# Kernel tuning notes

Hardware: AMD Instinct MI355X
Metric: run time of the kernel (lower is better)

## Reference

```python
import jax, jax.numpy as jnp
import numpy as np

E, H, FFN, NQ, NL = 1024, 16, 4096, 8, 4
LN_EPS = 1e-5


def _rx(t):
    c = jnp.cos(t / 2).astype(jnp.complex64)
    s = (-1j * jnp.sin(t / 2)).astype(jnp.complex64)
    return jnp.stack([jnp.stack([c, s]), jnp.stack([s, c])])


def _ry(t):
    c = jnp.cos(t / 2).astype(jnp.complex64)
    s = jnp.sin(t / 2).astype(jnp.complex64)
    return jnp.stack([jnp.stack([c, -s]), jnp.stack([s, c])])


def _rz(t):
    tc = t.astype(jnp.complex64)
    e0 = jnp.exp(-1j * tc / 2)
    e1 = jnp.exp(1j * tc / 2)
    z = jnp.zeros((), jnp.complex64)
    return jnp.stack([jnp.stack([e0, z]), jnp.stack([z, e1])])


def _apply_1q(state, gate, q):
    state = jnp.tensordot(gate, state, axes=([1], [q]))
    return jnp.moveaxis(state, 0, q)


def _cnot(state, c, t):
    s0, s1 = jnp.split(state, 2, axis=c)  # each keeps size-1 axis c
    s1 = jnp.flip(s1, axis=t)            # X on target when control=1
    return jnp.concatenate([s0, s1], axis=c)


def quantum_expvals(qparams):
    # statevector sim of the fixed (input-independent) variational circuit
    state = jnp.zeros((2,) * NQ, jnp.complex64).at[(0,) * NQ].set(1.0)
    for l in range(NL):
        for q in range(NQ):
            state = _apply_1q(state, _rx(qparams[l, q, 0]), q)
            state = _apply_1q(state, _ry(qparams[l, q, 1]), q)
            state = _apply_1q(state, _rz(qparams[l, q, 2]), q)
        for i in range(NQ - 1):
            state = _cnot(state, i, i + 1)
        state = _cnot(state, NQ - 1, 0)
    probs = jnp.abs(state) ** 2
    evs = [1.0 - 2.0 * jnp.sum(jnp.take(probs, 1, axis=q)) for q in range(NQ)]
    return jnp.stack(evs).astype(jnp.float32)  # [NQ]


def _layernorm(x, g, b):
    m = jnp.mean(x, axis=-1, keepdims=True)
    v = jnp.mean((x - m) ** 2, axis=-1, keepdims=True)
    return (x - m) / jnp.sqrt(v + LN_EPS) * g + b


def setup_inputs() -> dict:
    key = jax.random.key(0)
    ks = jax.random.split(key, 16)
    s = 1.0 / np.sqrt(E)
    inp = {
        "x": jax.random.normal(ks[0], (4, 1024, E), jnp.float32),
        "Wq": jax.random.normal(ks[1], (E, E), jnp.float32) * s,
        "Wk": jax.random.normal(ks[2], (E, E), jnp.float32) * s,
        "Wv": jax.random.normal(ks[3], (E, E), jnp.float32) * s,
        "Wo": jax.random.normal(ks[4], (E, E), jnp.float32) * s,
        "bo": jnp.zeros((E,), jnp.float32),
        "gate": jnp.ones((H,), jnp.float32),
        "g1": jnp.ones((E,), jnp.float32),
        "b1": jnp.zeros((E,), jnp.float32),
        "g2": jnp.ones((E,), jnp.float32),
        "b2": jnp.zeros((E,), jnp.float32),
        "Wi": jax.random.normal(ks[5], (NQ, E), jnp.float32) * s,
        "bi": jnp.zeros((NQ,), jnp.float32),
        "qparams": jax.random.normal(ks[6], (NL, NQ, 3), jnp.float32),
        "W1": jax.random.normal(ks[7], (FFN, NQ), jnp.float32) / np.sqrt(NQ),
        "bf1": jnp.zeros((FFN,), jnp.float32),
        "W2": jax.random.normal(ks[8], (E, FFN), jnp.float32) / np.sqrt(FFN),
        "bf2": jnp.zeros((E,), jnp.float32),
    }
    return inp


def reference(x, Wq, Wk, Wv, Wo, bo, gate, g1, b1, g2, b2, Wi, bi, qparams, W1, bf1, W2, bf2):
    B, T, _ = x.shape
    d_k = E // H
    # gated multi-head attention (dropout = identity / eval mode)
    q = (x @ Wq.T).reshape(B, T, H, d_k)
    k = (x @ Wk.T).reshape(B, T, H, d_k)
    v = (x @ Wv.T).reshape(B, T, H, d_k)
    scores = jnp.einsum("bqhd,bkhd->bhqk", q, k) / np.sqrt(d_k)
    attn = jax.nn.softmax(scores, axis=-1)
    out = jnp.einsum("bhqk,bkhd->bqhd", attn, v)
    out = out * jax.nn.sigmoid(gate)[None, None, :, None]
    attn_out = out.reshape(B, T, E) @ Wo.T + bo
    h = _layernorm(x + attn_out, g1, b1)
    # quantum FFN: input_linear output is computed but unused by the circuit
    h2d = h.reshape(B * T, E)
    _x_qubits = h2d @ Wi.T + bi  # faithfully computed, unused (as in original)
    evs = quantum_expvals(qparams)                      # [NQ], token-independent
    qout = jnp.broadcast_to(evs, (B * T, NQ))
    f = jax.nn.relu(qout @ W1.T + bf1) @ W2.T + bf2     # [B*T, E]
    ffn_out = f.reshape(B, T, E)
    return _layernorm(h + ffn_out, g2, b2)
```

## Files before the change

kernel.cpp:

```cpp
#include <hip/hip_runtime.h>

#define E_DIM 1024
#define SEQ 1024
#define BATCH 4
#define NHEAD 16
#define DK 64
#define TOK 4096
#define FFN_DIM 4096
#define NQB 8
#define NLAY 4

typedef __attribute__((ext_vector_type(8))) short short8;
typedef __attribute__((ext_vector_type(4))) float f32x4;
typedef unsigned short u16;
typedef unsigned int u32;

__device__ __forceinline__ u16 f2bf(float f) {
  union { float f; unsigned u; } v; v.f = f;
  unsigned r = v.u + 0x7fffu + ((v.u >> 16) & 1u);
  return (u16)(r >> 16);
}

__device__ __forceinline__ u32 cvtpk_bf16(float lo, float hi) {
  u32 r;
  asm("v_cvt_pk_bf16_f32 %0, %1, %2" : "=v"(r) : "v"(lo), "v"(hi));
  return r;
}

__device__ __forceinline__ void gload_lds16(const u16* g, u16* l) {
  __builtin_amdgcn_global_load_lds((const __attribute__((address_space(1))) unsigned int*)g,
                                   (__attribute__((address_space(3))) unsigned int*)l, 16, 0, 0);
}

__global__ void cast_kernel(const float* __restrict__ in, u16* __restrict__ out, int n4) {
  int i = blockIdx.x * blockDim.x + threadIdx.x;
  int stride = gridDim.x * blockDim.x;
  for (; i < n4; i += stride) {
    float4 v = ((const float4*)in)[i];
    ushort4 o;
    o.x = f2bf(v.x); o.y = f2bf(v.y); o.z = f2bf(v.z); o.w = f2bf(v.w);
    ((ushort4*)out)[i] = o;
  }
}

__global__ void cast4_kernel(const float* __restrict__ a0, const float* __restrict__ a1,
                             const float* __restrict__ a2, const float* __restrict__ a3,
                             u16* __restrict__ out, int n4per) {
  const float* src = blockIdx.z == 0 ? a0 : blockIdx.z == 1 ? a1 : blockIdx.z == 2 ? a2 : a3;
  u16* dst = out + (size_t)blockIdx.z * n4per * 4;
  int i = blockIdx.x * blockDim.x + threadIdx.x;
  int stride = gridDim.x * blockDim.x;
  for (; i < n4per; i += stride) {
    float4 v = ((const float4*)src)[i];
    ushort4 o;
    o.x = f2bf(v.x); o.y = f2bf(v.y); o.z = f2bf(v.z); o.w = f2bf(v.w);
    ((ushort4*)dst)[i] = o;
  }
}

template<int F32OUT, int ZTRANS>
__global__ __launch_bounds__(256) void gemm_bt(
    const u16* __restrict__ A,
    const u16* __restrict__ B0, const u16* __restrict__ B1, const u16* __restrict__ B2,
    void* __restrict__ C0, void* __restrict__ C1, void* __restrict__ C2,
    const float* __restrict__ bias, int K, int N) {
  const u16* B = blockIdx.z == 0 ? B0 : blockIdx.z == 1 ? B1 : B2;
  void* C = blockIdx.z == 0 ? C0 : blockIdx.z == 1 ? C1 : C2;
  __shared__ u16 As[128 * 32];
  __shared__ u16 Bs[128 * 32];
  const int tid = threadIdx.x;
  const int lane = tid & 63;
  const int wid = tid >> 6;
  const int wr = wid >> 1, wc = wid & 1;
  const int lr = lane & 15, lg = lane >> 4;
  const int row0 = blockIdx.y * 128;
  const int col0 = blockIdx.x * 128;
  const int ar = tid >> 2;
  const int ak = (tid & 3) * 8;
  const u16* Ag = A + (size_t)(row0 + ar) * K + ak;
  const u16* Bg = B + (size_t)(col0 + ar) * K + ak;
  u16* AsW = &As[wid * 512];
  u16* BsW = &Bs[wid * 512];
  f32x4 acc[4][4];
  const f32x4 fzero = {0.f, 0.f, 0.f, 0.f};
#pragma unroll
  for (int m = 0; m < 4; ++m)
#pragma unroll
    for (int n = 0; n < 4; ++n) acc[m][n] = fzero;
  for (int k0 = 0; k0 < K; k0 += 32) {
    __syncthreads();
    gload_lds16(Ag + k0, AsW);
    gload_lds16(Ag + (size_t)64 * K + k0, AsW + 2048);
    gload_lds16(Bg + k0, BsW);
    gload_lds16(Bg + (size_t)64 * K + k0, BsW + 2048);
    __syncthreads();
    short8 af[4], bfr[4];
#pragma unroll
    for (int m = 0; m < 4; ++m) af[m] = *(const short8*)&As[(wr * 64 + m * 16 + lr) * 32 + lg * 8];
#pragma unroll
    for (int n = 0; n < 4; ++n) bfr[n] = *(const short8*)&Bs[(wc * 64 + n * 16 + lr) * 32 + lg * 8];
#pragma unroll
    for (int m = 0; m < 4; ++m)
#pragma unroll
      for (int n = 0; n < 4; ++n)
        acc[m][n] = __builtin_amdgcn_mfma_f32_16x16x32_bf16(af[m], bfr[n], acc[m][n], 0, 0, 0);
  }
#pragma unroll
  for (int m = 0; m < 4; ++m) {
    const int growb = row0 + wr * 64 + m * 16 + lg * 4;
#pragma unroll
    for (int n = 0; n < 4; ++n) {
      const int gcol = col0 + wc * 64 + n * 16 + lr;
      if (ZTRANS >= 0 && blockIdx.z == ZTRANS) {
        ushort4 t4;
        t4.x = f2bf(acc[m][n][0]); t4.y = f2bf(acc[m][n][1]);
        t4.z = f2bf(acc[m][n][2]); t4.w = f2bf(acc[m][n][3]);
        *(ushort4*)&((u16*)C)[(size_t)gcol * TOK + growb] = t4;
      } else {
#pragma unroll
        for (int r = 0; r < 4; ++r) {
          size_t idx = (size_t)(growb + r) * N + gcol;
          if (F32OUT) ((float*)C)[idx] = acc[m][n][r] + bias[gcol];
          else ((u16*)C)[idx] = f2bf(acc[m][n][r]);
        }
      }
    }
  }
}

__global__ __launch_bounds__(256) void attn_kernel(
    const u16* __restrict__ qb, const u16* __restrict__ kb, const u16* __restrict__ vtb,
    const float* __restrict__ gate, u16* __restrict__ ob) {
  const int bid = blockIdx.x + (blockIdx.y << 4) + (blockIdx.z << 8);
  const int swz = (bid & 7) * 128 + (bid >> 3);
  const int qblk = swz & 15, h = (swz >> 4) & 15, b = swz >> 8;
  const int tid = threadIdx.x, lane = tid & 63, w = tid >> 6;
  const int lr = lane & 15, lg = lane >> 4;
  __shared__ u16 Kl[2][64 * 64];
  __shared__ u16 Vl[2][64 * 64];
  const u16* Qp = qb + (size_t)(b * SEQ + qblk * 64 + w * 16 + lr) * E_DIM + h * DK;
  const short8 bq0 = *(const short8*)&Qp[lg * 8];
  const short8 bq1 = *(const short8*)&Qp[32 + lg * 8];
  const int r0 = tid >> 3;
  const int cs = (tid & 7) ^ (r0 & 7);
  const u16* Kg0 = kb + (size_t)(b * SEQ + r0) * E_DIM + h * DK + cs * 8;
  const u16* Kg1 = Kg0 + (size_t)32 * E_DIM;
  const u16* Vg0 = vtb + (size_t)(h * DK + r0) * TOK + b * SEQ + cs * 8;
  const u16* Vg1 = Vg0 + (size_t)32 * TOK;
  const int ldsb = w * 512;
#define STAGE(bufi, kt) do { \
    const size_t ko = (size_t)(kt) * 64 * E_DIM; const int vo = (kt) * 64; \
    gload_lds16(Kg0 + ko, &Kl[bufi][ldsb]); \
    gload_lds16(Kg1 + ko, &Kl[bufi][2048 + ldsb]); \
    gload_lds16(Vg0 + vo, &Vl[bufi][ldsb]); \
    gload_lds16(Vg1 + vo, &Vl[bufi][2048 + ldsb]); \
  } while (0)
  f32x4 o[4];
  const f32x4 fzero = {0.f, 0.f, 0.f, 0.f};
#pragma unroll
  for (int dn = 0; dn < 4; ++dn) o[dn] = fzero;
  float mrun = -1e30f, lrun = 0.f;
  const int sw = (lr & 7) << 3;
  const int srcA = ((lg & 1) << 5) + lr;
  const bool hi = (lg & 2) != 0;
  STAGE(0, 0);
  __syncthreads();
  int cur = 0;
  for (int kt = 0; kt < 16; ++kt) {
    if (kt < 15) STAGE(cur ^ 1, kt + 1);
    const u16* Kc = Kl[cur];
    const u16* Vc = Vl[cur];
    f32x4 sT[4];
#pragma unroll
    for (int n = 0; n < 4; ++n) {
      const int base = (n * 16 + lr) * 64;
      const short8 ka0 = *(const short8*)&Kc[base + ((lg << 3) ^ sw)];
      const short8 ka1 = *(const short8*)&Kc[base + ((32 + (lg << 3)) ^ sw)];
      sT[n] = __builtin_amdgcn_mfma_f32_16x16x32_bf16(ka0, bq0, fzero, 0, 0, 0);
      sT[n] = __builtin_amdgcn_mfma_f32_16x16x32_bf16(ka1, bq1, sT[n], 0, 0, 0);
    }
    float mt = sT[0][0];
#pragma unroll
    for (int n = 0; n < 4; ++n)
#pragma unroll
      for (int r = 0; r < 4; ++r) mt = fmaxf(mt, sT[n][r]);
    mt = fmaxf(mt, __shfl_xor(mt, 16));
    mt = fmaxf(mt, __shfl_xor(mt, 32));
    const float mn = fmaxf(mrun, mt * 0.125f);
    const float alpha = __expf(mrun - mn);
    mrun = mn;
    float tsum = 0.f;
    u32 pk[4][2];
#pragma unroll
    for (int n = 0; n < 4; ++n) {
      const float p0 = __expf(sT[n][0] * 0.125f - mn);
      const float p1 = __expf(sT[n][1] * 0.125f - mn);
      const float p2 = __expf(sT[n][2] * 0.125f - mn);
      const float p3 = __expf(sT[n][3] * 0.125f - mn);
      tsum += (p0 + p1) + (p2 + p3);
      pk[n][0] = cvtpk_bf16(p0, p1);
      pk[n][1] = cvtpk_bf16(p2, p3);
    }
    tsum += __shfl_xor(tsum, 16);
    tsum += __shfl_xor(tsum, 32);
    lrun = lrun * alpha + tsum;
#pragma unroll
    for (int dn = 0; dn < 4; ++dn)
#pragma unroll
      for (int r = 0; r < 4; ++r) o[dn][r] *= alpha;
#pragma unroll
    for (int kh = 0; kh < 2; ++kh) {
      const int nb = kh * 2;
      union { short8 s8; u32 d[4]; } pf;
      const u32 a0 = (u32)__shfl((int)pk[nb][0], srcA);
      const u32 c0 = (u32)__shfl((int)pk[nb + 1][0], srcA);
      const u32 a1 = (u32)__shfl((int)pk[nb][1], srcA);
      const u32 c1 = (u32)__shfl((int)pk[nb + 1][1], srcA);
      const u32 a2 = (u32)__shfl((int)pk[nb][0], srcA + 16);
      const u32 c2 = (u32)__shfl((int)pk[nb + 1][0], srcA + 16);
      const u32 a3 = (u32)__shfl((int)pk[nb][1], srcA + 16);
      const u32 c3 = (u32)__shfl((int)pk[nb + 1][1], srcA + 16);
      pf.d[0] = hi ? c0 : a0;
      pf.d[1] = hi ? c1 : a1;
      pf.d[2] = hi ? c2 : a2;
      pf.d[3] = hi ? c3 : a3;
#pragma unroll
      for (int dn = 0; dn < 4; ++dn) {
        const int base = (dn * 16 + lr) * 64;
        const short8 va = *(const short8*)&Vc[base + ((((kh * 4 + lg) << 3)) ^ sw)];
        o[dn] = __builtin_amdgcn_mfma_f32_16x16x32_bf16(va, pf.s8, o[dn], 0, 0, 0);
      }
    }
    __syncthreads();
    cur ^= 1;
  }
  const float sg = 1.f / (1.f + __expf(-gate[h]));
  const float inv = sg / lrun;
  const size_t orow = (size_t)(b * SEQ + qblk * 64 + w * 16 + lr) * E_DIM + h * DK;
#pragma unroll
  for (int dn = 0; dn < 4; ++dn) {
    ushort4 o4;
    o4.x = f2bf(o[dn][0] * inv);
    o4.y = f2bf(o[dn][1] * inv);
    o4.z = f2bf(o[dn][2] * inv);
    o4.w = f2bf(o[dn][3] * inv);
    *(ushort4*)&ob[orow + dn * 16 + lg * 4] = o4;
  }
#undef STAGE
}

__global__ __launch_bounds__(256) void quantum_kernel(
    const float* __restrict__ qparams, const float* __restrict__ W1,
    const float* __restrict__ bf1, float* __restrict__ relu_out) {
  __shared__ float csl[96], snl[96];
  __shared__ float evs_s[NQB];
  const int t = threadIdx.x;
  if (t < NLAY * NQB * 3) {
    const float th = qparams[t] * 0.5f;
    csl[t] = cosf(th);
    snl[t] = sinf(th);
  }
  __syncthreads();
  if (t < 64) {
    const int lane = t;
    float2 a[4];
    a[0] = make_float2(lane == 0 ? 1.f : 0.f, 0.f);
    a[1] = make_float2(0.f, 0.f);
    a[2] = make_float2(0.f, 0.f);
    a[3] = make_float2(0.f, 0.f);
#pragma unroll
    for (int l = 0; l < NLAY; ++l) {
#pragma unroll
      for (int q = 0; q < NQB; ++q) {
        const int pi = (l * NQB + q) * 3;
        const float cx = csl[pi],     sx = snl[pi];
        const float cy = csl[pi + 1], sy = snl[pi + 1];
        const float cz = csl[pi + 2], sz = snl[pi + 2];
        if (q < 6) {
          const int m = 1 << (5 - q);
          const int b = (lane >> (5 - q)) & 1;
#pragma unroll
          for (int r = 0; r < 4; ++r) {
            const float px = __shfl_xor(a[r].x, m);
            const float py = __shfl_xor(a[r].y, m);
            a[r] = make_float2(cx * a[r].x + sx * py, cx * a[r].y - sx * px);
          }
          const float sgy = b ? sy : -sy;
#pragma unroll
          for (int r = 0; r < 4; ++r) {
            const float px = __shfl_xor(a[r].x, m);
            const float py = __shfl_xor(a[r].y, m);
            a[r] = make_float2(cy * a[r].x + sgy * px, cy * a[r].y + sgy * py);
          }
          const float sgz = b ? -sz : sz;
#pragma unroll
          for (int r = 0; r < 4; ++r)
            a[r] = make_float2(cz * a[r].x + sgz * a[r].y, cz * a[r].y - sgz * a[r].x);
        } else if (q == 6) {
#pragma unroll
          for (int r = 0; r < 2; ++r) {
            float2 lo = a[r], hiv = a[r + 2];
            a[r]     = make_float2(cx * lo.x + sx * hiv.y, cx * lo.y - sx * hiv.x);
            a[r + 2] = make_float2(cx * hiv.x + sx * lo.y, cx * hiv.y - sx * lo.x);
          }
#pragma unroll
          for (int r = 0; r < 2; ++r) {
            float2 lo = a[r], hiv = a[r + 2];
            a[r]     = make_float2(cy * lo.x - sy * hiv.x, cy * lo.y - sy * hiv.y);
            a[r + 2] = make_float2(sy * lo.x + cy * hiv.x, sy * lo.y + cy * hiv.y);
          }
#pragma unroll
          for (int r = 0; r < 2; ++r) {
            float2 lo = a[r], hiv = a[r + 2];
            a[r]     = make_float2(cz * lo.x + sz * lo.y, cz * lo.y - sz * lo.x);
            a[r + 2] = make_float2(cz * hiv.x - sz * hiv.y, cz * hiv.y + sz * hiv.x);
          }
        } else {
#pragma unroll
          for (int r = 0; r < 4; r += 2) {
            float2 lo = a[r], hiv = a[r + 1];
            a[r]     = make_float2(cx * lo.x + sx * hiv.y, cx * lo.y - sx * hiv.x);
            a[r + 1] = make_float2(cx * hiv.x + sx * lo.y, cx * hiv.y - sx * lo.x);
          }
#pragma unroll
          for (int r = 0; r < 4; r += 2) {
            float2 lo = a[r], hiv = a[r + 1];
            a[r]     = make_float2(cy * lo.x - sy * hiv.x, cy * lo.y - sy * hiv.y);
            a[r + 1] = make_float2(sy * lo.x + cy * hiv.x, sy * lo.y + cy * hiv.y);
          }
#pragma unroll
          for (int r = 0; r < 4; r += 2) {
            float2 lo = a[r], hiv = a[r + 1];
            a[r]     = make_float2(cz * lo.x + sz * lo.y, cz * lo.y - sz * lo.x);
            a[r + 1] = make_float2(cz * hiv.x - sz * hiv.y, cz * hiv.y + sz * hiv.x);
          }
        }
      }
#pragma unroll
      for (int i = 0; i < 5; ++i) {
        const int cbit = 5 - i;
        const int tmask = 1 << (4 - i);
        const int ctrl = (lane >> cbit) & 1;
#pragma unroll
        for (int r = 0; r < 4; ++r) {
          const float px = __shfl_xor(a[r].x, tmask);
          const float py = __shfl_xor(a[r].y, tmask);
          if (ctrl) a[r] = make_float2(px, py);
        }
      }
      if (lane & 1) {
        float2 t0 = a[0]; a[0] = a[2]; a[2] = t0;
        float2 t1 = a[1]; a[1] = a[3]; a[3] = t1;
      }
      { float2 tt = a[2]; a[2] = a[3]; a[3] = tt; }
      a[1].x = __shfl_xor(a[1].x, 32); a[1].y = __shfl_xor(a[1].y, 32);
      a[3].x = __shfl_xor(a[3].x, 32); a[3].y = __shfl_xor(a[3].y, 32);
    }
    const float p0 = a[0].x * a[0].x + a[0].y * a[0].y;
    const float p1 = a[1].x * a[1].x + a[1].y * a[1].y;
    const float p2 = a[2].x * a[2].x + a[2].y * a[2].y;
    const float p3 = a[3].x * a[3].x + a[3].y * a[3].y;
    const float ptot = (p0 + p1) + (p2 + p3);
    float ev[8];
#pragma unroll
    for (int q = 0; q < 6; ++q) ev[q] = ((lane >> (5 - q)) & 1) ? ptot : 0.f;
    ev[6] = p2 + p3;
    ev[7] = p1 + p3;
#pragma unroll
    for (int d = 1; d < 64; d <<= 1)
#pragma unroll
      for (int q = 0; q < 8; ++q) ev[q] += __shfl_xor(ev[q], d);
    if (lane == 0) {
#pragma unroll
      for (int q = 0; q < 8; ++q) evs_s[q] = 1.f - 2.f * ev[q];
    }
  }
  __syncthreads();
  float e0 = evs_s[0], e1 = evs_s[1], e2 = evs_s[2], e3 = evs_s[3];
  float e4 = evs_s[4], e5 = evs_s[5], e6 = evs_s[6], e7 = evs_s[7];
  for (int j = t; j < FFN_DIM; j += 256) {
    const float4 w0 = *(const float4*)&W1[j * NQB];
    const float4 w1 = *(const float4*)&W1[j * NQB + 4];
    float acc = bf1[j];
    acc += e0 * w0.x + e1 * w0.y + e2 * w0.z + e3 * w0.w;
    acc += e4 * w1.x + e5 * w1.y + e6 * w1.z + e7 * w1.w;
    relu_out[j] = fmaxf(acc, 0.f);
  }
}

__global__ __launch_bounds__(256) void fvec_kernel(
    const float* __restrict__ W2, const float* __restrict__ bf2,
    const float* __restrict__ relu_vec, float* __restrict__ fvec) {
  const int w = threadIdx.x >> 6, lane = threadIdx.x & 63;
  const int e = blockIdx.x * 4 + w;
  const float* row = W2 + (size_t)e * FFN_DIM;
  float s = 0.f;
  for (int i = lane * 4; i < FFN_DIM; i += 256) {
    const float4 wv = *(const float4*)&row[i];
    const float4 rv = *(const float4*)&relu_vec[i];
    s += wv.x * rv.x + wv.y * rv.y + wv.z * rv.z + wv.w * rv.w;
  }
#pragma unroll
  for (int d = 32; d >= 1; d >>= 1) s += __shfl_down(s, d);
  if (lane == 0) fvec[e] = s + bf2[e];
}

__global__ __launch_bounds__(256) void final_ln_kernel(
    const float* __restrict__ x, const float* __restrict__ ao, const float* __restrict__ fvec,
    const float* __restrict__ g1, const float* __restrict__ b1,
    const float* __restrict__ g2, const float* __restrict__ b2, float* __restrict__ out) {
  __shared__ float sm1[8];
  __shared__ float sm2[8];
  const size_t row = blockIdx.x;
  const int tid = threadIdx.x;
  const int w = tid >> 6, lane = tid & 63;
  const float4 xv = *(const float4*)&x[row * E_DIM + tid * 4];
  const float4 av = *(const float4*)&ao[row * E_DIM + tid * 4];
  float v0 = xv.x + av.x, v1 = xv.y + av.y, v2 = xv.z + av.z, v3 = xv.w + av.w;
  float s = v0 + v1 + v2 + v3;
  float ss = v0 * v0 + v1 * v1 + v2 * v2 + v3 * v3;
#pragma unroll
  for (int d = 32; d >= 1; d >>= 1) { s += __shfl_down(s, d); ss += __shfl_down(ss, d); }
  if (lane == 0) { sm1[w * 2] = s; sm1[w * 2 + 1] = ss; }
  __syncthreads();
  s = sm1[0] + sm1[2] + sm1[4] + sm1[6];
  ss = sm1[1] + sm1[3] + sm1[5] + sm1[7];
  const float mean = s * (1.f / 1024.f);
  const float var = ss * (1.f / 1024.f) - mean * mean;
  const float rstd = rsqrtf(var + 1e-5f);
  const float4 g1v = *(const float4*)&g1[tid * 4];
  const float4 b1v = *(const float4*)&b1[tid * 4];
  const float4 fv = *(const float4*)&fvec[tid * 4];
  float z0 = (v0 - mean) * rstd * g1v.x + b1v.x + fv.x;
  float z1 = (v1 - mean) * rstd * g1v.y + b1v.y + fv.y;
  float z2 = (v2 - mean) * rstd * g1v.z + b1v.z + fv.z;
  float z3 = (v3 - mean) * rstd * g1v.w + b1v.w + fv.w;
  float s2 = z0 + z1 + z2 + z3;
  float ss2 = z0 * z0 + z1 * z1 + z2 * z2 + z3 * z3;
#pragma unroll
  for (int d = 32; d >= 1; d >>= 1) { s2 += __shfl_down(s2, d); ss2 += __shfl_down(ss2, d); }
  if (lane == 0) { sm2[w * 2] = s2; sm2[w * 2 + 1] = ss2; }
  __syncthreads();
  s2 = sm2[0] + sm2[2] + sm2[4] + sm2[6];
  ss2 = sm2[1] + sm2[3] + sm2[5] + sm2[7];
  const float mean2 = s2 * (1.f / 1024.f);
  const float var2 = ss2 * (1.f / 1024.f) - mean2 * mean2;
  const float rstd2 = rsqrtf(var2 + 1e-5f);
  const float4 g2v = *(const float4*)&g2[tid * 4];
  const float4 b2v = *(const float4*)&b2[tid * 4];
  float4 ov;
  ov.x = (z0 - mean2) * rstd2 * g2v.x + b2v.x;
  ov.y = (z1 - mean2) * rstd2 * g2v.y + b2v.y;
  ov.z = (z2 - mean2) * rstd2 * g2v.z + b2v.z;
  ov.w = (z3 - mean2) * rstd2 * g2v.w + b2v.w;
  *(float4*)&out[row * E_DIM + tid * 4] = ov;
}

extern "C" void kernel_launch(void* const* d_in, const int* in_sizes, int n_in,
                              void* d_out, int out_size, void* d_ws, size_t ws_size,
                              hipStream_t stream) {
  (void)in_sizes; (void)n_in; (void)out_size; (void)ws_size;
  const float* x       = (const float*)d_in[0];
  const float* Wq      = (const float*)d_in[1];
  const float* Wk      = (const float*)d_in[2];
  const float* Wv      = (const float*)d_in[3];
  const float* Wo      = (const float*)d_in[4];
  const float* bo      = (const float*)d_in[5];
  const float* gate    = (const float*)d_in[6];
  const float* g1      = (const float*)d_in[7];
  const float* b1      = (const float*)d_in[8];
  const float* g2      = (const float*)d_in[9];
  const float* b2      = (const float*)d_in[10];
  const float* qparams = (const float*)d_in[13];
  const float* W1      = (const float*)d_in[14];
  const float* bf1     = (const float*)d_in[15];
  const float* W2      = (const float*)d_in[16];
  const float* bf2     = (const float*)d_in[17];

  char* ws = (char*)d_ws;
  u16* xb        = (u16*)(ws + 0);
  u16* wqb       = (u16*)(ws + 8388608);
  u16* wkb       = (u16*)(ws + 10485760);
  u16* wvb       = (u16*)(ws + 12582912);
  u16* wob       = (u16*)(ws + 14680064);
  u16* qb        = (u16*)(ws + 16777216);
  u16* kb        = (u16*)(ws + 25165824);
  u16* vtb       = (u16*)(ws + 33554432);
  u16* ab        = (u16*)(ws + 41943040);
  float* ao      = (float*)(ws + 50331648);
  float* relu_vec= (float*)(ws + 67108864);
  float* fvec    = (float*)(ws + 67125248);

  cast_kernel<<<2048, 256, 0, stream>>>(x, xb, TOK * E_DIM / 4);
  cast4_kernel<<<dim3(1024, 1, 4), 256, 0, stream>>>(Wq, Wk, Wv, Wo, wqb, E_DIM * E_DIM / 4);
  quantum_kernel<<<1, 256, 0, stream>>>(qparams, W1, bf1, relu_vec);
  fvec_kernel<<<256, 256, 0, stream>>>(W2, bf2, relu_vec, fvec);
  gemm_bt<0, 2><<<dim3(8, 32, 3), 256, 0, stream>>>(xb, wqb, wkb, wvb, qb, kb, vtb, nullptr, E_DIM, E_DIM);
  attn_kernel<<<dim3(16, 16, 4), 256, 0, stream>>>(qb, kb, vtb, gate, ab);
  gemm_bt<1, -1><<<dim3(8, 32, 1), 256, 0, stream>>>(ab, wob, wob, wob, ao, ao, ao, bo, E_DIM, E_DIM);
  final_ln_kernel<<<4096, 256, 0, stream>>>(x, ao, fvec, g1, b1, g2, b2, (float*)d_out);
}
```

Baseline: 253.0 us.

## Merge cast kernels and fuse quantum sim with FFN vector into one kernel

Combines the activation cast and the four weight casts into one grid-stride kernel. It also folds the quantum circuit simulation, the W1 relu vector and the W2 matvec into a single 256-block kernel. Each block redundantly recomputes the statevector and the relu vector into shared memory before computing its four output elements. This cuts two kernel launches and the serial single-block stage, at the cost of redundant per-block simulation work (loops now not unrolled) and an extra shared-memory array.

```diff
diff --git a/kernel.cpp b/kernel.cpp
--- a/kernel.cpp
+++ b/kernel.cpp
@@ -32,29 +32,29 @@
                                    (__attribute__((address_space(3))) unsigned int*)l, 16, 0, 0);
 }
 
-__global__ void cast_kernel(const float* __restrict__ in, u16* __restrict__ out, int n4) {
+__global__ __launch_bounds__(256) void cast_all_kernel(
+    const float* __restrict__ x, const float* __restrict__ Wq, const float* __restrict__ Wk,
+    const float* __restrict__ Wv, const float* __restrict__ Wo,
+    u16* __restrict__ xb, u16* __restrict__ wqb) {
+  const int NX = TOK * E_DIM / 4;
+  const int NW = E_DIM * E_DIM / 4;
+  const int total = NX + 4 * NW;
   int i = blockIdx.x * blockDim.x + threadIdx.x;
-  int stride = gridDim.x * blockDim.x;
-  for (; i < n4; i += stride) {
-    float4 v = ((const float4*)in)[i];
+  const int stride = gridDim.x * blockDim.x;
+  for (; i < total; i += stride) {
+    const float* src; u16* dst; int idx;
+    if (i < NX) { src = x; dst = xb; idx = i; }
+    else {
+      const int j = i - NX;
+      const int wsel = j / NW;
+      idx = j - wsel * NW;
+      src = wsel == 0 ? Wq : wsel == 1 ? Wk : wsel == 2 ? Wv : Wo;
+      dst = wqb + (size_t)wsel * (E_DIM * E_DIM);
+    }
+    const float4 v = ((const float4*)src)[idx];
     ushort4 o;
     o.x = f2bf(v.x); o.y = f2bf(v.y); o.z = f2bf(v.z); o.w = f2bf(v.w);
-    ((ushort4*)out)[i] = o;
-  }
-}
-
-__global__ void cast4_kernel(const float* __restrict__ a0, const float* __restrict__ a1,
-                             const float* __restrict__ a2, const float* __restrict__ a3,
-                             u16* __restrict__ out, int n4per) {
-  const float* src = blockIdx.z == 0 ? a0 : blockIdx.z == 1 ? a1 : blockIdx.z == 2 ? a2 : a3;
-  u16* dst = out + (size_t)blockIdx.z * n4per * 4;
-  int i = blockIdx.x * blockDim.x + threadIdx.x;
-  int stride = gridDim.x * blockDim.x;
-  for (; i < n4per; i += stride) {
-    float4 v = ((const float4*)src)[i];
-    ushort4 o;
-    o.x = f2bf(v.x); o.y = f2bf(v.y); o.z = f2bf(v.z); o.w = f2bf(v.w);
-    ((ushort4*)dst)[i] = o;
+    ((ushort4*)dst)[idx] = o;
   }
 }
 
@@ -249,11 +249,13 @@
 #undef STAGE
 }
 
-__global__ __launch_bounds__(256) void quantum_kernel(
+__global__ __launch_bounds__(256) void qffn_kernel(
     const float* __restrict__ qparams, const float* __restrict__ W1,
-    const float* __restrict__ bf1, float* __restrict__ relu_out) {
+    const float* __restrict__ bf1, const float* __restrict__ W2,
+    const float* __restrict__ bf2, float* __restrict__ fvec) {
   __shared__ float csl[96], snl[96];
   __shared__ float evs_s[NQB];
+  __shared__ float relu_s[FFN_DIM];
   const int t = threadIdx.x;
   if (t < NLAY * NQB * 3) {
     const float th = qparams[t] * 0.5f;
@@ -268,9 +270,9 @@
     a[1] = make_float2(0.f, 0.f);
     a[2] = make_float2(0.f, 0.f);
     a[3] = make_float2(0.f, 0.f);
-#pragma unroll
+#pragma unroll 1
     for (int l = 0; l < NLAY; ++l) {
-#pragma unroll
+#pragma unroll 1
       for (int q = 0; q < NQB; ++q) {
         const int pi = (l * NQB + q) * 3;
         const float cx = csl[pi],     sx = snl[pi];
@@ -336,11 +338,10 @@
           }
         }
       }
-#pragma unroll
+#pragma unroll 1
       for (int i = 0; i < 5; ++i) {
-        const int cbit = 5 - i;
         const int tmask = 1 << (4 - i);
-        const int ctrl = (lane >> cbit) & 1;
+        const int ctrl = (lane >> (5 - i)) & 1;
 #pragma unroll
         for (int r = 0; r < 4; ++r) {
           const float px = __shfl_xor(a[r].x, tmask);
@@ -366,7 +367,7 @@
     for (int q = 0; q < 6; ++q) ev[q] = ((lane >> (5 - q)) & 1) ? ptot : 0.f;
     ev[6] = p2 + p3;
     ev[7] = p1 + p3;
-#pragma unroll
+#pragma unroll 1
     for (int d = 1; d < 64; d <<= 1)
 #pragma unroll
       for (int q = 0; q < 8; ++q) ev[q] += __shfl_xor(ev[q], d);
@@ -376,28 +377,24 @@
     }
   }
   __syncthreads();
-  float e0 = evs_s[0], e1 = evs_s[1], e2 = evs_s[2], e3 = evs_s[3];
-  float e4 = evs_s[4], e5 = evs_s[5], e6 = evs_s[6], e7 = evs_s[7];
+  const float e0 = evs_s[0], e1 = evs_s[1], e2 = evs_s[2], e3 = evs_s[3];
+  const float e4 = evs_s[4], e5 = evs_s[5], e6 = evs_s[6], e7 = evs_s[7];
   for (int j = t; j < FFN_DIM; j += 256) {
     const float4 w0 = *(const float4*)&W1[j * NQB];
     const float4 w1 = *(const float4*)&W1[j * NQB + 4];
     float acc = bf1[j];
     acc += e0 * w0.x + e1 * w0.y + e2 * w0.z + e3 * w0.w;
     acc += e4 * w1.x + e5 * w1.y + e6 * w1.z + e7 * w1.w;
-    relu_out[j] = fmaxf(acc, 0.f);
-  }
-}
-
-__global__ __launch_bounds__(256) void fvec_kernel(
-    const float* __restrict__ W2, const float* __restrict__ bf2,
-    const float* __restrict__ relu_vec, float* __restrict__ fvec) {
-  const int w = threadIdx.x >> 6, lane = threadIdx.x & 63;
-  const int e = blockIdx.x * 4 + w;
+    relu_s[j] = fmaxf(acc, 0.f);
+  }
+  __syncthreads();
+  const int lane = t & 63;
+  const int e = blockIdx.x * 4 + (t >> 6);
   const float* row = W2 + (size_t)e * FFN_DIM;
   float s = 0.f;
   for (int i = lane * 4; i < FFN_DIM; i += 256) {
     const float4 wv = *(const float4*)&row[i];
-    const float4 rv = *(const float4*)&relu_vec[i];
+    const float4 rv = *(const float4*)&relu_s[i];
     s += wv.x * rv.x + wv.y * rv.y + wv.z * rv.z + wv.w * rv.w;
   }
 #pragma unroll
@@ -480,21 +477,18 @@
   char* ws = (char*)d_ws;
   u16* xb        = (u16*)(ws + 0);
   u16* wqb       = (u16*)(ws + 8388608);
-  u16* wkb       = (u16*)(ws + 10485760);
-  u16* wvb       = (u16*)(ws + 12582912);
-  u16* wob       = (u16*)(ws + 14680064);
   u16* qb        = (u16*)(ws + 16777216);
   u16* kb        = (u16*)(ws + 25165824);
   u16* vtb       = (u16*)(ws + 33554432);
   u16* ab        = (u16*)(ws + 41943040);
   float* ao      = (float*)(ws + 50331648);
-  float* relu_vec= (float*)(ws + 67108864);
-  float* fvec    = (float*)(ws + 67125248);
-
-  cast_kernel<<<2048, 256, 0, stream>>>(x, xb, TOK * E_DIM / 4);
-  cast4_kernel<<<dim3(1024, 1, 4), 256, 0, stream>>>(Wq, Wk, Wv, Wo, wqb, E_DIM * E_DIM / 4);
-  quantum_kernel<<<1, 256, 0, stream>>>(qparams, W1, bf1, relu_vec);
-  fvec_kernel<<<256, 256, 0, stream>>>(W2, bf2, relu_vec, fvec);
+  float* fvec    = (float*)(ws + 67108864);
+  u16* wkb = wqb + E_DIM * E_DIM;
+  u16* wvb = wkb + E_DIM * E_DIM;
+  u16* wob = wvb + E_DIM * E_DIM;
+
+  cast_all_kernel<<<2048, 256, 0, stream>>>(x, Wq, Wk, Wv, Wo, xb, wqb);
+  qffn_kernel<<<256, 256, 0, stream>>>(qparams, W1, bf1, W2, bf2, fvec);
   gemm_bt<0, 2><<<dim3(8, 32, 3), 256, 0, stream>>>(xb, wqb, wkb, wvb, qb, kb, vtb, nullptr, E_DIM, E_DIM);
   attn_kernel<<<dim3(16, 16, 4), 256, 0, stream>>>(qb, kb, vtb, gate, ab);
   gemm_bt<1, -1><<<dim3(8, 32, 1), 256, 0, stream>>>(ab, wob, wob, wob, ao, ao, ao, bo, E_DIM, E_DIM);
```

Measured after the change: 256.7 us (median of 2 runs). Within noise of the previous version (+1.5%).
